# Performance work log

Hardware: AMD Instinct MI355X
Metric: run time of the kernel (lower is better)

## Reference

```python
import jax, jax.numpy as jnp
import numpy as np

N_NODES = 100000
N_EDGES = 3200000
D_IN = 128
D_OUT = 128


def setup_inputs() -> dict:
    key = jax.random.key(0)
    k1, k2, k3, k4, k5 = jax.random.split(key, 5)
    x = jax.random.normal(k1, (N_NODES, D_IN), dtype=jnp.float32)
    edge_index = jax.random.randint(k2, (2, N_EDGES), 0, N_NODES, dtype=jnp.int64)
    edge_weight = jax.random.uniform(k3, (N_EDGES,), dtype=jnp.float32)
    W = jax.random.normal(k4, (D_IN, D_OUT), dtype=jnp.float32) / np.sqrt(D_IN)
    b = jax.random.normal(k5, (D_OUT,), dtype=jnp.float32)
    return {"x": x, "edge_index": edge_index, "edge_weight": edge_weight, "W": W, "b": b}


def reference(x, edge_index, edge_weight, W, b):
    # GCNConv: add self-loops (weight 1), symmetric deg^{-1/2} normalization,
    # linear transform, scatter-add aggregation source -> target, + bias.
    N = x.shape[0]
    src, dst = edge_index[0], edge_index[1]
    loops = jnp.arange(N, dtype=edge_index.dtype)
    src_f = jnp.concatenate([src, loops])
    dst_f = jnp.concatenate([dst, loops])
    w_f = jnp.concatenate([edge_weight, jnp.ones((N,), dtype=edge_weight.dtype)])
    # degree over target nodes (PyG gcn_norm with flow source_to_target)
    deg = jax.ops.segment_sum(w_f, dst_f, num_segments=N)
    deg_inv_sqrt = jnp.where(deg > 0, jax.lax.rsqrt(deg), 0.0)
    norm = deg_inv_sqrt[src_f] * w_f * deg_inv_sqrt[dst_f]  # [E+N]
    h = x @ W  # [N, D_OUT]
    msgs = h[src_f] * norm[:, None]  # gather + scale, [E+N, D_OUT]
    out = jax.ops.segment_sum(msgs, dst_f, num_segments=N)  # scatter-add
    return out + b
```

## Files before the change

### kernel.cpp

```cpp
#include <hip/hip_runtime.h>

#define NN 100000
#define NE 3200000
#define D  128
#define NBUCK 782
#define EPB 2048
#define NBLK ((NE + EPB - 1) / EPB)

typedef __attribute__((ext_vector_type(8))) short bf16x8;
typedef __attribute__((ext_vector_type(4))) float f32x4;
typedef __attribute__((ext_vector_type(2))) float f32x2;

__device__ __forceinline__ float bf2f(unsigned int u) {
    union { unsigned int i; float f; } v; v.i = u << 16; return v.f;
}
__device__ __forceinline__ float bits2f(unsigned int u) {
    union { unsigned int i; float f; } v; v.i = u; return v.f;
}
__device__ __forceinline__ unsigned int f2bf(float f) {
    union { float f; unsigned int i; } v; v.f = f;
    unsigned int u = v.i;
    return (u + 0x7fffu + ((u >> 16) & 1u)) >> 16;
}

__global__ __launch_bounds__(1024) void zero_detect_kernel(const int* __restrict__ ei,
        int* __restrict__ flag, int* __restrict__ gcnt) {
    int t = threadIdx.x;
    if (t < NBUCK) gcnt[t] = 0;
    if (t < 64) {
        int v = ei[2 * t + 1];
        unsigned long long ball = __ballot(v != 0);
        if (t == 0) flag[0] = (ball == 0ull) ? 1 : 0;
    }
}

__global__ __launch_bounds__(256) void count1_kernel(const int* __restrict__ ei,
        int* __restrict__ gcnt, unsigned short* __restrict__ blockbase,
        const int* __restrict__ flag) {
    __shared__ int h[NBUCK];
    int t = threadIdx.x, b = blockIdx.x;
    int s = flag[0];
    for (int j = t; j < NBUCK; j += 256) h[j] = 0;
    __syncthreads();
    long e0 = (long)b * EPB;
#pragma unroll
    for (int it = 0; it < EPB / 256; ++it) {
        long e = e0 + it * 256 + t;
        if (e < NE) {
            int d = s ? (int)((const long*)ei)[NE + e] : ei[NE + e];
            atomicAdd(&h[d >> 7], 1);
        }
    }
    __syncthreads();
    for (int j = t; j < NBUCK; j += 256) {
        int v = h[j];
        unsigned short bb = 0;
        if (v) bb = (unsigned short)atomicAdd(&gcnt[j], v);
        blockbase[(size_t)b * NBUCK + j] = bb;
    }
}

__global__ __launch_bounds__(1024) void scanb_kernel(const int* __restrict__ gcnt,
        int* __restrict__ gbase) {
    __shared__ int s[1024];
    int t = threadIdx.x;
    s[t] = (t < NBUCK) ? gcnt[t] : 0;
    __syncthreads();
    for (int off = 1; off < 1024; off <<= 1) {
        int v = (t >= off) ? s[t - off] : 0;
        __syncthreads();
        s[t] += v;
        __syncthreads();
    }
    if (t < NBUCK) gbase[t] = (t > 0) ? s[t - 1] : 0;
    if (t == 0) gbase[NBUCK] = NE;
}

__global__ __launch_bounds__(256) void scatter1_kernel(const int* __restrict__ ei,
        const float* __restrict__ ew, const int* __restrict__ gbase,
        const unsigned short* __restrict__ blockbase, const int* __restrict__ flag,
        unsigned long long* __restrict__ tmp) {
    __shared__ int gb[NBUCK];
    __shared__ unsigned short bbs[NBUCK];
    __shared__ int cur[NBUCK];
    int t = threadIdx.x, b = blockIdx.x;
    int s = flag[0];
    for (int j = t; j < NBUCK; j += 256) {
        gb[j] = gbase[j];
        bbs[j] = blockbase[(size_t)b * NBUCK + j];
        cur[j] = 0;
    }
    __syncthreads();
    long e0 = (long)b * EPB;
#pragma unroll
    for (int it = 0; it < EPB / 256; ++it) {
        long e = e0 + it * 256 + t;
        if (e < NE) {
            int src, dst;
            if (s) { src = (int)((const long*)ei)[e]; dst = (int)((const long*)ei)[NE + e]; }
            else   { src = ei[e];                     dst = ei[NE + e]; }
            float w = ew[e];
            int bkt = dst >> 7, dlow = dst & 127;
            int r = atomicAdd(&cur[bkt], 1);
            unsigned int word = ((unsigned int)src << 15) | (f2bf(w) >> 1);
            tmp[gb[bkt] + (int)bbs[bkt] + r] =
                ((unsigned long long)(unsigned int)dlow << 32) | word;
        }
    }
}

__global__ __launch_bounds__(256) void build2_kernel(const unsigned long long* __restrict__ tmp,
        const int* __restrict__ gbase, int* __restrict__ row_ptr, unsigned int* __restrict__ csr,
        float* __restrict__ dis) {
    __shared__ int hist[128], excl[128], cur[128];
    __shared__ float wsum[128];
    int t = threadIdx.x, k = blockIdx.x;
    int base = gbase[k], endb = gbase[k + 1];
    if (t < 128) { hist[t] = 0; cur[t] = 0; wsum[t] = 0.f; }
    __syncthreads();
    for (int i = base + t; i < endb; i += 256) {
        unsigned long long v = tmp[i];
        int dl = (int)(v >> 32);
        atomicAdd(&hist[dl], 1);
        atomicAdd(&wsum[dl], bf2f(((unsigned int)v & 0x7fffu) << 1));
    }
    __syncthreads();
    if (t < 128) excl[t] = hist[t];
    __syncthreads();
    for (int off = 1; off < 128; off <<= 1) {
        int v = (t >= off && t < 128) ? excl[t - off] : 0;
        __syncthreads();
        if (t < 128) excl[t] += v;
        __syncthreads();
    }
    if (t < 128) {
        int ex = excl[t] - hist[t];
        int node = k * 128 + t;
        if (node < NN) {
            row_ptr[node] = base + ex;
            dis[node] = rsqrtf(1.0f + wsum[t]);
        }
        if (node == NN - 1) row_ptr[NN] = NE;
        excl[t] = ex;
    }
    __syncthreads();
    for (int i = base + t; i < endb; i += 256) {
        unsigned long long v = tmp[i];
        int dl = (int)(v >> 32);
        int r = atomicAdd(&cur[dl], 1);
        csr[base + excl[dl] + r] = (unsigned int)v;
    }
}

__global__ __launch_bounds__(256) void mgemm_kernel(const float* __restrict__ x,
        const float* __restrict__ W, const float* __restrict__ dis,
        unsigned short* __restrict__ hb) {
    __shared__ unsigned short WT[16 * 128 * 8];
    int t = threadIdx.x;
    {
        int n = t & 127, half = t >> 7;
        for (int it = 0; it < 8; ++it) {
            int kb = half * 8 + it;
            union { unsigned short s[8]; uint4 v; } pk;
#pragma unroll
            for (int j = 0; j < 8; ++j)
                pk.s[j] = (unsigned short)f2bf(W[(kb * 8 + j) * D + n]);
            *(uint4*)&WT[(kb * 128 + n) * 8] = pk.v;
        }
    }
    __syncthreads();
    int l = t & 63, w = t >> 6;
    int q = l >> 4, m = l & 15;
    long mbase = (long)blockIdx.x * 128 + w * 32;
    long r0 = mbase + m;      if (r0 > NN - 1) r0 = NN - 1;
    long r1 = mbase + 16 + m; if (r1 > NN - 1) r1 = NN - 1;
    const float* a0p = x + r0 * D + q * 8;
    const float* a1p = x + r1 * D + q * 8;
    f32x4 acc[2][8];
#pragma unroll
    for (int mt = 0; mt < 2; ++mt)
#pragma unroll
        for (int nt = 0; nt < 8; ++nt) acc[mt][nt] = (f32x4){0.f, 0.f, 0.f, 0.f};
#pragma unroll
    for (int kc = 0; kc < 4; ++kc) {
        float4 va0 = *(const float4*)(a0p + kc * 32);
        float4 va1 = *(const float4*)(a0p + kc * 32 + 4);
        float4 vb0 = *(const float4*)(a1p + kc * 32);
        float4 vb1 = *(const float4*)(a1p + kc * 32 + 4);
        union { unsigned short s[8]; bf16x8 v; } ua, ub;
        ua.s[0] = (unsigned short)f2bf(va0.x); ua.s[1] = (unsigned short)f2bf(va0.y);
        ua.s[2] = (unsigned short)f2bf(va0.z); ua.s[3] = (unsigned short)f2bf(va0.w);
        ua.s[4] = (unsigned short)f2bf(va1.x); ua.s[5] = (unsigned short)f2bf(va1.y);
        ua.s[6] = (unsigned short)f2bf(va1.z); ua.s[7] = (unsigned short)f2bf(va1.w);
        ub.s[0] = (unsigned short)f2bf(vb0.x); ub.s[1] = (unsigned short)f2bf(vb0.y);
        ub.s[2] = (unsigned short)f2bf(vb0.z); ub.s[3] = (unsigned short)f2bf(vb0.w);
        ub.s[4] = (unsigned short)f2bf(vb1.x); ub.s[5] = (unsigned short)f2bf(vb1.y);
        ub.s[6] = (unsigned short)f2bf(vb1.z); ub.s[7] = (unsigned short)f2bf(vb1.w);
        const bf16x8* bp = (const bf16x8*)WT + (kc * 4 + q) * 128 + m;
#pragma unroll
        for (int nt = 0; nt < 8; ++nt) {
            bf16x8 bfr = bp[nt * 16];
            acc[0][nt] = __builtin_amdgcn_mfma_f32_16x16x32_bf16(ua.v, bfr, acc[0][nt], 0, 0, 0);
            acc[1][nt] = __builtin_amdgcn_mfma_f32_16x16x32_bf16(ub.v, bfr, acc[1][nt], 0, 0, 0);
        }
    }
#pragma unroll
    for (int mt = 0; mt < 2; ++mt) {
        long rowbase = mbase + mt * 16;
#pragma unroll
        for (int r = 0; r < 4; ++r) {
            long row = rowbase + q * 4 + r;
            float dsc = dis[(row < NN) ? row : (NN - 1)];
#pragma unroll
            for (int nt = 0; nt < 8; ++nt)
                if (row < NN)
                    hb[row * D + nt * 16 + m] = (unsigned short)f2bf(acc[mt][nt][r] * dsc);
        }
    }
}

__global__ __launch_bounds__(256) void pull_kernel(const unsigned int* __restrict__ hb,
        const float* __restrict__ dis, const int* __restrict__ row_ptr,
        const unsigned int* __restrict__ csr, const float2* __restrict__ bias2,
        float* __restrict__ out) {
    int t = blockIdx.x * 256 + threadIdx.x;
    int n = t >> 6, l = t & 63;
    float dn = dis[n];
    unsigned int a = hb[n * 64 + l];
    float accx = bits2f(a << 16);
    float accy = bits2f(a & 0xffff0000u);
    int e = row_ptr[n], end = row_ptr[n + 1];
    for (; e + 7 < end; e += 8) {
        unsigned int c[8];
#pragma unroll
        for (int j = 0; j < 8; ++j) c[j] = __builtin_nontemporal_load(csr + e + j);
        int s_[8];
#pragma unroll
        for (int j = 0; j < 8; ++j) s_[j] = c[j] >> 15;
        unsigned int u[8];
#pragma unroll
        for (int j = 0; j < 8; ++j) u[j] = hb[s_[j] * 64 + l];
#pragma unroll
        for (int j = 0; j < 8; ++j) {
            float m = bits2f(c[j] << 17);
            accx += bits2f(u[j] << 16) * m;
            accy += bits2f(u[j] & 0xffff0000u) * m;
        }
    }
    for (; e + 1 < end; e += 2) {
        unsigned int c0 = __builtin_nontemporal_load(csr + e);
        unsigned int c1 = __builtin_nontemporal_load(csr + e + 1);
        int s0 = c0 >> 15, s1 = c1 >> 15;
        unsigned int u0 = hb[s0 * 64 + l];
        unsigned int u1 = hb[s1 * 64 + l];
        float m0 = bits2f(c0 << 17), m1 = bits2f(c1 << 17);
        accx += bits2f(u0 << 16) * m0; accy += bits2f(u0 & 0xffff0000u) * m0;
        accx += bits2f(u1 << 16) * m1; accy += bits2f(u1 & 0xffff0000u) * m1;
    }
    if (e < end) {
        unsigned int c0 = __builtin_nontemporal_load(csr + e);
        int s0 = c0 >> 15;
        unsigned int u0 = hb[s0 * 64 + l];
        float m0 = bits2f(c0 << 17);
        accx += bits2f(u0 << 16) * m0; accy += bits2f(u0 & 0xffff0000u) * m0;
    }
    float2 bv = bias2[l];
    f32x2 r;
    r.x = accx * dn + bv.x;
    r.y = accy * dn + bv.y;
    __builtin_nontemporal_store(r, (f32x2*)out + ((size_t)n * 64 + l));
}

extern "C" void kernel_launch(void* const* d_in, const int* in_sizes, int n_in,
                              void* d_out, int out_size, void* d_ws, size_t ws_size,
                              hipStream_t stream) {
    const float* x  = (const float*)d_in[0];
    const int*   ei = (const int*)d_in[1];
    const float* ew = (const float*)d_in[2];
    const float* W  = (const float*)d_in[3];
    const float* b  = (const float*)d_in[4];
    float* out = (float*)d_out;

    unsigned long long* tmp = (unsigned long long*)d_ws;
    unsigned short*     hb  = (unsigned short*)d_ws;
    unsigned int*       csr = (unsigned int*)((char*)d_ws + (size_t)NE * 8);
    float*              dis = (float*)(csr + NE);
    int*            row_ptr = (int*)(dis + NN);
    int*            gcnt    = row_ptr + NN + 1;
    int*            gbase   = gcnt + NBUCK;
    int*            flag    = gbase + NBUCK + 1;
    unsigned short* blockbase = (unsigned short*)(flag + 1);

    zero_detect_kernel<<<1, 1024, 0, stream>>>(ei, flag, gcnt);
    count1_kernel<<<NBLK, 256, 0, stream>>>(ei, gcnt, blockbase, flag);
    scanb_kernel<<<1, 1024, 0, stream>>>(gcnt, gbase);
    scatter1_kernel<<<NBLK, 256, 0, stream>>>(ei, ew, gbase, blockbase, flag, tmp);
    build2_kernel<<<NBUCK, 256, 0, stream>>>(tmp, gbase, row_ptr, csr, dis);
    mgemm_kernel<<<(NN + 127) / 128, 256, 0, stream>>>(x, W, dis, hb);
    pull_kernel<<<(NN * 64) / 256, 256, 0, stream>>>((const unsigned int*)hb, dis, row_ptr, csr,
                                                     (const float2*)b, (float*)out);
}
```

Baseline: 442.5 us.

## Use wider 256-node buckets and stage bucket segments in shared memory

Buckets now cover 256 destination nodes instead of 128, and each counting/scatter block handles 8192 edges, so there are fewer buckets and fewer blocks. build2 copies each bucket's edge records into a 72KB shared buffer on the first pass and reads them back from there on the second pass, instead of reading global memory twice, with a global fallback when a bucket is too large. In exchange, build2 occupancy drops because of the large LDS footprint, fewer blocks run in parallel, and the 16-bit per-block offsets in blockbase must still fit.

```diff
diff --git a/kernel.cpp b/kernel.cpp
--- a/kernel.cpp
+++ b/kernel.cpp
@@ -3,9 +3,10 @@
 #define NN 100000
 #define NE 3200000
 #define D  128
-#define NBUCK 782
-#define EPB 2048
+#define NBUCK 391
+#define EPB 8192
 #define NBLK ((NE + EPB - 1) / EPB)
+#define BCAP 9216
 
 typedef __attribute__((ext_vector_type(8))) short bf16x8;
 typedef __attribute__((ext_vector_type(4))) float f32x4;
@@ -23,7 +24,7 @@
     return (u + 0x7fffu + ((u >> 16) & 1u)) >> 16;
 }
 
-__global__ __launch_bounds__(1024) void zero_detect_kernel(const int* __restrict__ ei,
+__global__ __launch_bounds__(512) void zero_detect_kernel(const int* __restrict__ ei,
         int* __restrict__ flag, int* __restrict__ gcnt) {
     int t = threadIdx.x;
     if (t < NBUCK) gcnt[t] = 0;
@@ -48,25 +49,23 @@
         long e = e0 + it * 256 + t;
         if (e < NE) {
             int d = s ? (int)((const long*)ei)[NE + e] : ei[NE + e];
-            atomicAdd(&h[d >> 7], 1);
+            atomicAdd(&h[d >> 8], 1);
         }
     }
     __syncthreads();
     for (int j = t; j < NBUCK; j += 256) {
-        int v = h[j];
-        unsigned short bb = 0;
-        if (v) bb = (unsigned short)atomicAdd(&gcnt[j], v);
-        blockbase[(size_t)b * NBUCK + j] = bb;
-    }
-}
-
-__global__ __launch_bounds__(1024) void scanb_kernel(const int* __restrict__ gcnt,
+        int bb = atomicAdd(&gcnt[j], h[j]);
+        blockbase[(size_t)b * NBUCK + j] = (unsigned short)bb;
+    }
+}
+
+__global__ __launch_bounds__(512) void scanb_kernel(const int* __restrict__ gcnt,
         int* __restrict__ gbase) {
-    __shared__ int s[1024];
+    __shared__ int s[512];
     int t = threadIdx.x;
     s[t] = (t < NBUCK) ? gcnt[t] : 0;
     __syncthreads();
-    for (int off = 1; off < 1024; off <<= 1) {
+    for (int off = 1; off < 512; off <<= 1) {
         int v = (t >= off) ? s[t - off] : 0;
         __syncthreads();
         s[t] += v;
@@ -100,7 +99,7 @@
             if (s) { src = (int)((const long*)ei)[e]; dst = (int)((const long*)ei)[NE + e]; }
             else   { src = ei[e];                     dst = ei[NE + e]; }
             float w = ew[e];
-            int bkt = dst >> 7, dlow = dst & 127;
+            int bkt = dst >> 8, dlow = dst & 255;
             int r = atomicAdd(&cur[bkt], 1);
             unsigned int word = ((unsigned int)src << 15) | (f2bf(w) >> 1);
             tmp[gb[bkt] + (int)bbs[bkt] + r] =
@@ -112,43 +111,63 @@
 __global__ __launch_bounds__(256) void build2_kernel(const unsigned long long* __restrict__ tmp,
         const int* __restrict__ gbase, int* __restrict__ row_ptr, unsigned int* __restrict__ csr,
         float* __restrict__ dis) {
-    __shared__ int hist[128], excl[128], cur[128];
-    __shared__ float wsum[128];
+    __shared__ unsigned long long seg[BCAP];
+    __shared__ int hist[256], excl[256], cur[256];
+    __shared__ float wsum[256];
     int t = threadIdx.x, k = blockIdx.x;
     int base = gbase[k], endb = gbase[k + 1];
-    if (t < 128) { hist[t] = 0; cur[t] = 0; wsum[t] = 0.f; }
-    __syncthreads();
-    for (int i = base + t; i < endb; i += 256) {
-        unsigned long long v = tmp[i];
-        int dl = (int)(v >> 32);
-        atomicAdd(&hist[dl], 1);
-        atomicAdd(&wsum[dl], bf2f(((unsigned int)v & 0x7fffu) << 1));
-    }
-    __syncthreads();
-    if (t < 128) excl[t] = hist[t];
-    __syncthreads();
-    for (int off = 1; off < 128; off <<= 1) {
-        int v = (t >= off && t < 128) ? excl[t - off] : 0;
+    int cnt = endb - base;
+    hist[t] = 0; cur[t] = 0; wsum[t] = 0.f;
+    __syncthreads();
+    if (cnt <= BCAP) {
+        for (int i = t; i < cnt; i += 256) {
+            unsigned long long v = tmp[base + i];
+            seg[i] = v;
+            int dl = (int)(v >> 32);
+            atomicAdd(&hist[dl], 1);
+            atomicAdd(&wsum[dl], bf2f(((unsigned int)v & 0x7fffu) << 1));
+        }
+    } else {
+        for (int i = base + t; i < endb; i += 256) {
+            unsigned long long v = tmp[i];
+            int dl = (int)(v >> 32);
+            atomicAdd(&hist[dl], 1);
+            atomicAdd(&wsum[dl], bf2f(((unsigned int)v & 0x7fffu) << 1));
+        }
+    }
+    __syncthreads();
+    excl[t] = hist[t];
+    __syncthreads();
+    for (int off = 1; off < 256; off <<= 1) {
+        int v = (t >= off) ? excl[t - off] : 0;
         __syncthreads();
-        if (t < 128) excl[t] += v;
+        excl[t] += v;
         __syncthreads();
     }
-    if (t < 128) {
-        int ex = excl[t] - hist[t];
-        int node = k * 128 + t;
-        if (node < NN) {
-            row_ptr[node] = base + ex;
-            dis[node] = rsqrtf(1.0f + wsum[t]);
-        }
-        if (node == NN - 1) row_ptr[NN] = NE;
-        excl[t] = ex;
-    }
-    __syncthreads();
-    for (int i = base + t; i < endb; i += 256) {
-        unsigned long long v = tmp[i];
-        int dl = (int)(v >> 32);
-        int r = atomicAdd(&cur[dl], 1);
-        csr[base + excl[dl] + r] = (unsigned int)v;
+    int ex = excl[t] - hist[t];
+    int node = k * 256 + t;
+    if (node < NN) {
+        row_ptr[node] = base + ex;
+        dis[node] = rsqrtf(1.0f + wsum[t]);
+    }
+    if (node == NN - 1) row_ptr[NN] = NE;
+    __syncthreads();
+    excl[t] = ex;
+    __syncthreads();
+    if (cnt <= BCAP) {
+        for (int i = t; i < cnt; i += 256) {
+            unsigned long long v = seg[i];
+            int dl = (int)(v >> 32);
+            int r = atomicAdd(&cur[dl], 1);
+            csr[base + excl[dl] + r] = (unsigned int)v;
+        }
+    } else {
+        for (int i = base + t; i < endb; i += 256) {
+            unsigned long long v = tmp[i];
+            int dl = (int)(v >> 32);
+            int r = atomicAdd(&cur[dl], 1);
+            csr[base + excl[dl] + r] = (unsigned int)v;
+        }
     }
 }
 
@@ -291,9 +310,9 @@
     int*            flag    = gbase + NBUCK + 1;
     unsigned short* blockbase = (unsigned short*)(flag + 1);
 
-    zero_detect_kernel<<<1, 1024, 0, stream>>>(ei, flag, gcnt);
+    zero_detect_kernel<<<1, 512, 0, stream>>>(ei, flag, gcnt);
     count1_kernel<<<NBLK, 256, 0, stream>>>(ei, gcnt, blockbase, flag);
-    scanb_kernel<<<1, 1024, 0, stream>>>(gcnt, gbase);
+    scanb_kernel<<<1, 512, 0, stream>>>(gcnt, gbase);
     scatter1_kernel<<<NBLK, 256, 0, stream>>>(ei, ew, gbase, blockbase, flag, tmp);
     build2_kernel<<<NBUCK, 256, 0, stream>>>(tmp, gbase, row_ptr, csr, dis);
     mgemm_kernel<<<(NN + 127) / 128, 256, 0, stream>>>(x, W, dis, hb);
```

Measured after the change: 374.5 us. 1.18x faster.
